# Kernel tuning notes

Measured on AMD Instinct MI355X. Metric: run time of the kernel, lower is better.

## Reference

```python
import jax, jax.numpy as jnp
import numpy as np

B, L, P, K, D, H = 8192, 224, 6, 5, 128, 4
S = K * K                 # 25 spatial positions in the patch
CENTER = S // 2           # central target pixel index
SCALE_RANGE = 0.2
BN_EPS = 1e-5


def _uniform(k, shape, fan_in):
    s = 1.0 / np.sqrt(fan_in)
    return jax.random.uniform(k, shape, jnp.float32, -s, s)


def setup_inputs() -> dict:
    key = jax.random.key(0)
    ks = jax.random.split(key, 32)
    inp = {}
    inp["x"] = jax.random.normal(ks[0], (B, L, K, K), jnp.float32)
    # attention projections (stored as (in, out), applied as x @ W + b)
    inp["wk_w"] = _uniform(ks[1], (L, D), L); inp["wk_b"] = _uniform(ks[2], (D,), L)
    inp["wv_w"] = _uniform(ks[3], (L, D), L); inp["wv_b"] = _uniform(ks[4], (D,), L)
    inp["wq_w"] = _uniform(ks[5], (L, D), L); inp["wq_b"] = _uniform(ks[6], (D,), L)
    inp["ng_w"] = _uniform(ks[7], (D, 1), D); inp["ng_b"] = _uniform(ks[8], (1,), D)
    # ffn branch: GLU(128->64) -> BN -> GLU(64->P)
    inp["f1_fw"] = _uniform(ks[9], (D, 64), D);  inp["f1_fb"] = _uniform(ks[10], (64,), D)
    inp["f1_gw"] = _uniform(ks[11], (D, 64), D); inp["f1_gb"] = _uniform(ks[12], (64,), D)
    inp["f_bn_g"] = jnp.ones((64,), jnp.float32); inp["f_bn_b"] = jnp.zeros((64,), jnp.float32)
    inp["f2_fw"] = _uniform(ks[13], (64, P), 64); inp["f2_fb"] = _uniform(ks[14], (P,), 64)
    inp["f2_gw"] = _uniform(ks[15], (64, P), 64); inp["f2_gb"] = _uniform(ks[16], (P,), 64)
    # scalar branch: same shapes
    inp["s1_fw"] = _uniform(ks[17], (D, 64), D);  inp["s1_fb"] = _uniform(ks[18], (64,), D)
    inp["s1_gw"] = _uniform(ks[19], (D, 64), D);  inp["s1_gb"] = _uniform(ks[20], (64,), D)
    inp["s_bn_g"] = jnp.ones((64,), jnp.float32); inp["s_bn_b"] = jnp.zeros((64,), jnp.float32)
    inp["s2_fw"] = _uniform(ks[21], (64, P), 64); inp["s2_fb"] = _uniform(ks[22], (P,), 64)
    inp["s2_gw"] = _uniform(ks[23], (64, P), 64); inp["s2_gb"] = _uniform(ks[24], (P,), 64)
    # endmember spectra (P, L), nonnegative as typical for HSI
    inp["endmember"] = jax.random.uniform(ks[25], (P, L), jnp.float32)
    return inp


def _swish(x):
    return x * jax.nn.sigmoid(x)


def _glu(x, fw, fb, gw, gb):
    return (x @ fw + fb) * jax.nn.sigmoid(x @ gw + gb)


def _bn_train(x, g, b):
    # BatchNorm1d training-mode forward: biased batch stats over batch dim
    m = jnp.mean(x, axis=0)
    v = jnp.var(x, axis=0)
    return (x - m) * jax.lax.rsqrt(v + BN_EPS) * g + b


def _forward(x, wk_w, wk_b, wv_w, wv_b, wq_w, wq_b, ng_w, ng_b,
             f1_fw, f1_fb, f1_gw, f1_gb, f_bn_g, f_bn_b, f2_fw, f2_fb, f2_gw, f2_gb,
             s1_fw, s1_fb, s1_gw, s1_gb, s_bn_g, s_bn_b, s2_fw, s2_fb, s2_gw, s2_gb,
             endmember):
    b = x.shape[0]
    xt = x.reshape(b, L, S).transpose(0, 2, 1)        # (B, S, L)
    keys = xt @ wk_w + wk_b                            # (B, S, D)
    vals = xt @ wv_w + wv_b                            # (B, S, D)
    q = xt[:, CENTER] @ wq_w + wq_b                    # (B, D)
    dk, dv = D // H, D // H
    kh = keys.reshape(b, S, H, dk)
    qh = q.reshape(b, H, dk)
    # note: scaling uses full key_dim (np.sqrt(self.key_dim)), not per-head dim
    scores = jnp.einsum('bhd,bshd->bhs', qh, kh) / np.sqrt(D).astype(np.float32)
    mask = jnp.zeros((S,), jnp.float32).at[CENTER].set(-1e6)
    att = jax.nn.softmax(scores + mask, axis=-1)       # (B, H, S)
    vh = vals.reshape(b, S, H, dv)
    surround = jnp.einsum('bhs,bshd->bhd', att, vh).reshape(b, D)
    central = vals[:, CENTER]                          # (B, D)
    nearby = jax.nn.sigmoid((central - surround) @ ng_w + ng_b)  # (B, 1)
    ss = central + nearby * surround                   # (B, D) spatial-spectral feature

    h = _glu(_swish(ss), f1_fw, f1_fb, f1_gw, f1_gb)
    h = _swish(_bn_train(h, f_bn_g, f_bn_b))
    abd = jax.nn.softmax(_glu(h, f2_fw, f2_fb, f2_gw, f2_gb), axis=1)  # (B, P)

    g = _glu(_swish(ss), s1_fw, s1_fb, s1_gw, s1_gb)
    g = _swish(_bn_train(g, s_bn_g, s_bn_b))
    edm_scale = jnp.tanh(_glu(g, s2_fw, s2_fb, s2_gw, s2_gb))          # (B, P)

    scale = 1.0 + SCALE_RANGE * edm_scale[:, :, None]  # (B, P, 1)
    edm = scale * endmember[None]                      # (B, P, L)
    recon = jnp.einsum('bp,bpl->bl', abd, edm)         # (B, L)
    return recon, abd, edm_scale


def reference(x, wk_w, wk_b, wv_w, wv_b, wq_w, wq_b, ng_w, ng_b,
              f1_fw, f1_fb, f1_gw, f1_gb, f_bn_g, f_bn_b, f2_fw, f2_fb, f2_gw, f2_gb,
              s1_fw, s1_fb, s1_gw, s1_gb, s_bn_g, s_bn_b, s2_fw, s2_fb, s2_gw, s2_gb,
              endmember):
    return _forward(x, wk_w, wk_b, wv_w, wv_b, wq_w, wq_b, ng_w, ng_b,
                    f1_fw, f1_fb, f1_gw, f1_gb, f_bn_g, f_bn_b, f2_fw, f2_fb, f2_gw, f2_gb,
                    s1_fw, s1_fb, s1_gw, s1_gb, s_bn_g, s_bn_b, s2_fw, s2_fb, s2_gw, s2_gb,
                    endmember)
```

## Files before the change

kernel.cpp:

```cpp
#include <hip/hip_runtime.h>
#include <hip/hip_bf16.h>

typedef unsigned short ushort;
typedef unsigned int   uint;
typedef __bf16 bfrag_t __attribute__((ext_vector_type(8)));
typedef float  ffrag_t __attribute__((ext_vector_type(4)));

#define NB   8192
#define LL   224
#define SS   25
#define CTR  12
#define DD   128
#define PP   6
#define HID  64
#define GPB  2
#define NKC  7
#define NMT  4
#define NNT  24
#define VST  132
#define WPK_ELEMS (NKC * NNT * 64 * 8)
#define FC1_ELEMS (4 * 16 * 64 * 8)

__device__ __forceinline__ float f_sigmoid(float x) { return 1.0f / (1.0f + __expf(-x)); }
__device__ __forceinline__ ushort f2bf(float f) {
    __hip_bfloat16 h = __float2bfloat16(f);
    ushort u; __builtin_memcpy(&u, &h, 2); return u;
}
__device__ __forceinline__ float bfu2f(ushort u) {
    uint v = ((uint)u) << 16; float f; __builtin_memcpy(&f, &v, 4); return f;
}

__global__ __launch_bounds__(256) void k0_pack(
    const float* __restrict__ wk_w, const float* __restrict__ wv_w,
    const float* __restrict__ wq_w,
    const float* __restrict__ f1_fw, const float* __restrict__ f1_gw,
    const float* __restrict__ s1_fw, const float* __restrict__ s1_gw,
    ushort* __restrict__ wpack, ushort* __restrict__ fc1pack)
{
    const int blk = blockIdx.x;
    if (blk < NNT) {
        const int nt  = blk;
        const int mat = nt >> 3;
        const float* w = mat == 0 ? wk_w : (mat == 1 ? wv_w : wq_w);
        const int cb = (nt & 7) * 16;
        for (int e = threadIdx.x; e < NKC * 64 * 8; e += 256) {
            int j    = e & 7;
            int lane = (e >> 3) & 63;
            int kc   = e >> 9;
            int k = kc * 32 + ((lane >> 4) << 3) + j;
            int c = cb + (lane & 15);
            wpack[((kc * NNT + nt) * 64 + lane) * 8 + j] = f2bf(w[k * DD + c]);
        }
    } else {
        const int nt = blk - NNT;
        const int m2 = nt >> 2;
        const float* w = m2 == 0 ? f1_fw : (m2 == 1 ? f1_gw : (m2 == 2 ? s1_fw : s1_gw));
        const int cb = (nt & 3) * 16;
        for (int e = threadIdx.x; e < 4 * 64 * 8; e += 256) {
            int j    = e & 7;
            int lane = (e >> 3) & 63;
            int kc   = e >> 9;
            int k = kc * 32 + ((lane >> 4) << 3) + j;
            int c = cb + (lane & 15);
            fc1pack[((kc * 16 + nt) * 64 + lane) * 8 + j] = f2bf(w[k * HID + c]);
        }
    }
}

__global__ __launch_bounds__(512, 4) void kA_front(
    const float* __restrict__ x,
    const ushort* __restrict__ wpack,
    const float* __restrict__ wk_b, const float* __restrict__ wv_b,
    const float* __restrict__ wq_b,
    const float* __restrict__ ng_w, const float* __restrict__ ng_b,
    ushort* __restrict__ swv_ws)
{
    __shared__ ushort alds[NMT * NKC * 64 * 8];
    __shared__ float  qv[GPB * DD];
    __shared__ float  att[8 * 26];
    __shared__ float  red[4];

    const int t    = threadIdx.x;
    const int b0   = blockIdx.x * GPB;
    const int wave = t >> 6;
    const int lane = t & 63;

    for (int g = 0; g < GPB; ++g) {
        const float* xb = x + (size_t)(b0 + g) * (LL * SS);
        for (int i = t; i < LL * SS; i += 512) {
            int l = i / SS;
            int s = i - l * SS;
            int r  = g * 32 + s;
            int idx = (((r >> 4) * NKC + (l >> 5)) * 64 +
                       ((r & 15) | (((l >> 3) & 3) << 4))) * 8 + (l & 7);
            alds[idx] = f2bf(xb[i]);
        }
    }
    __syncthreads();

    ffrag_t acck[NMT], accv[NMT], accq[2];
#pragma unroll
    for (int mt = 0; mt < NMT; ++mt) {
        acck[mt] = ffrag_t{0.f, 0.f, 0.f, 0.f};
        accv[mt] = ffrag_t{0.f, 0.f, 0.f, 0.f};
    }
    accq[0] = ffrag_t{0.f, 0.f, 0.f, 0.f};
    accq[1] = ffrag_t{0.f, 0.f, 0.f, 0.f};

    for (int kc = 0; kc < NKC; ++kc) {
        bfrag_t bk = *(const bfrag_t*)(wpack + ((kc * NNT + wave) * 64 + lane) * 8);
        bfrag_t bv = *(const bfrag_t*)(wpack + ((kc * NNT + wave + 8) * 64 + lane) * 8);
        bfrag_t bq = *(const bfrag_t*)(wpack + ((kc * NNT + wave + 16) * 64 + lane) * 8);
#pragma unroll
        for (int mt = 0; mt < NMT; ++mt) {
            bfrag_t af = *(const bfrag_t*)(alds + ((mt * NKC + kc) * 64 + lane) * 8);
            acck[mt] = __builtin_amdgcn_mfma_f32_16x16x32_bf16(af, bk, acck[mt], 0, 0, 0);
            accv[mt] = __builtin_amdgcn_mfma_f32_16x16x32_bf16(af, bv, accv[mt], 0, 0, 0);
            if ((mt & 1) == 0)
                accq[mt >> 1] = __builtin_amdgcn_mfma_f32_16x16x32_bf16(af, bq, accq[mt >> 1], 0, 0, 0);
        }
    }
    __syncthreads();

    {
        const int c  = wave * 16 + (lane & 15);
        const float bk = wk_b[c];
        const float bv = wv_b[c];
#pragma unroll
        for (int mt = 0; mt < NMT; ++mt) {
#pragma unroll
            for (int reg = 0; reg < 4; ++reg) {
                int r = mt * 16 + ((lane >> 4) << 2) + reg;
                int g = r >> 5;
                int s = r & 31;
                if (s < SS) {
                    alds[(g * SS + s) * VST + c]        = f2bf(acck[mt][reg] + bk);
                    alds[6600 + (g * SS + s) * VST + c] = f2bf(accv[mt][reg] + bv);
                }
            }
        }
        if ((lane >> 4) == 3) {
            float bq = wq_b[c];
            qv[c]      = accq[0][0] + bq;
            qv[DD + c] = accq[1][0] + bq;
        }
    }
    __syncthreads();

    if (t < 256) {
        const int r   = t >> 5;
        const int g   = r >> 2;
        const int h   = r & 3;
        const int l32 = t & 31;
        float sc = -1e30f;
        if (l32 < SS) {
            const ushort* kr = alds + (g * SS + l32) * VST + h * 32;
            const float*  qr = qv + g * DD + h * 32;
            float a0 = 0.f, a1 = 0.f, a2 = 0.f, a3 = 0.f;
#pragma unroll
            for (int i = 0; i < 32; i += 4) {
                a0 = fmaf(qr[i + 0], bfu2f(kr[i + 0]), a0);
                a1 = fmaf(qr[i + 1], bfu2f(kr[i + 1]), a1);
                a2 = fmaf(qr[i + 2], bfu2f(kr[i + 2]), a2);
                a3 = fmaf(qr[i + 3], bfu2f(kr[i + 3]), a3);
            }
            sc = ((a0 + a1) + (a2 + a3)) * 0.088388347648318447f;
            if (l32 == CTR) sc -= 1e6f;
        }
        float mx = sc;
#pragma unroll
        for (int m = 16; m > 0; m >>= 1) mx = fmaxf(mx, __shfl_xor(mx, m, 32));
        float e = __expf(sc - mx);
        float sum = e;
#pragma unroll
        for (int m = 16; m > 0; m >>= 1) sum += __shfl_xor(sum, m, 32);
        if (l32 < SS) att[r * 26 + l32] = e / sum;
    }
    __syncthreads();

    if (t < 256) {
        const int g = t >> 7;
        const int d = t & 127;
        const int h = d >> 5;
        const ushort* vrow = alds + 6600 + g * SS * VST + d;
        const float* arow = att + (g * 4 + h) * 26;
        float s0 = 0.f, s1 = 0.f;
#pragma unroll
        for (int s = 0; s < 24; s += 2) {
            s0 = fmaf(arow[s],     bfu2f(vrow[s * VST]),       s0);
            s1 = fmaf(arow[s + 1], bfu2f(vrow[(s + 1) * VST]), s1);
        }
        float sur = fmaf(arow[24], bfu2f(vrow[24 * VST]), s0 + s1);
        float cen = bfu2f(vrow[CTR * VST]);
        float term = (cen - sur) * ng_w[d];
#pragma unroll
        for (int off = 32; off > 0; off >>= 1) term += __shfl_down(term, off);
        if (lane == 0) red[wave] = term;
        __syncthreads();
        float tot = red[g * 2] + red[g * 2 + 1] + ng_b[0];
        float nearby = f_sigmoid(tot);
        float ssv = cen + nearby * sur;
        float sw  = ssv * f_sigmoid(ssv);
        swv_ws[(size_t)(b0 + g) * DD + d] = f2bf(sw);
    } else {
        __syncthreads();
    }
}

__global__ __launch_bounds__(256) void kC_fc1(
    const ushort* __restrict__ swv_ws,
    const ushort* __restrict__ fc1pack,
    const float* __restrict__ f1_fb, const float* __restrict__ f1_gb,
    const float* __restrict__ s1_fb, const float* __restrict__ s1_gb,
    float* __restrict__ h1_ws, float* __restrict__ g1_ws)
{
    const int t    = threadIdx.x;
    const int wave = t >> 6;
    const int lane = t & 63;
    const int m0   = blockIdx.x * 32;

    ffrag_t acc[4][2];
#pragma unroll
    for (int ni = 0; ni < 4; ++ni)
#pragma unroll
        for (int mt = 0; mt < 2; ++mt) acc[ni][mt] = ffrag_t{0.f, 0.f, 0.f, 0.f};

#pragma unroll
    for (int kc = 0; kc < 4; ++kc) {
        bfrag_t bf[4];
#pragma unroll
        for (int ni = 0; ni < 4; ++ni) {
            int nt = wave + 4 * ni;
            bf[ni] = *(const bfrag_t*)(fc1pack + ((kc * 16 + nt) * 64 + lane) * 8);
        }
#pragma unroll
        for (int mt = 0; mt < 2; ++mt) {
            bfrag_t af = *(const bfrag_t*)(swv_ws +
                (size_t)(m0 + mt * 16 + (lane & 15)) * DD + kc * 32 + ((lane >> 4) << 3));
#pragma unroll
            for (int ni = 0; ni < 4; ++ni)
                acc[ni][mt] = __builtin_amdgcn_mfma_f32_16x16x32_bf16(af, bf[ni], acc[ni][mt], 0, 0, 0);
        }
    }

    const int c16 = wave * 16 + (lane & 15);
    const float fb1 = f1_fb[c16], gb1 = f1_gb[c16];
    const float fb2 = s1_fb[c16], gb2 = s1_gb[c16];
#pragma unroll
    for (int mt = 0; mt < 2; ++mt) {
#pragma unroll
        for (int reg = 0; reg < 4; ++reg) {
            int m = m0 + mt * 16 + ((lane >> 4) << 2) + reg;
            float hf = acc[0][mt][reg] + fb1;
            float hg = acc[1][mt][reg] + gb1;
            float gf = acc[2][mt][reg] + fb2;
            float gg = acc[3][mt][reg] + gb2;
            h1_ws[(size_t)m * HID + c16] = hf * f_sigmoid(hg);
            g1_ws[(size_t)m * HID + c16] = gf * f_sigmoid(gg);
        }
    }
}

__global__ __launch_bounds__(256) void k2a_part(
    const float* __restrict__ h1, const float* __restrict__ g1,
    float* __restrict__ part)
{
    const int br    = blockIdx.x >> 5;
    const int chunk = blockIdx.x & 31;
    const float* src = br ? g1 : h1;
    const int t = threadIdx.x;
    const int w = t >> 6;
    const int j = t & 63;
    const int base = chunk * 256;
    float s = 0.f, sq = 0.f;
    for (int i = 0; i < 64; ++i) {
        float v = src[(size_t)(base + i * 4 + w) * HID + j];
        s += v;
        sq = fmaf(v, v, sq);
    }
    __shared__ float ls[4][64], lq[4][64];
    ls[w][j] = s; lq[w][j] = sq;
    __syncthreads();
    if (t < 64) {
        float S = ls[0][t] + ls[1][t] + ls[2][t] + ls[3][t];
        float Q = lq[0][t] + lq[1][t] + lq[2][t] + lq[3][t];
        float* pr = part + (br * 32 + chunk) * 128;
        pr[t]      = S;
        pr[64 + t] = Q;
    }
}

__global__ __launch_bounds__(128) void k2b_fin(
    const float* __restrict__ part,
    const float* __restrict__ fg, const float* __restrict__ fb,
    const float* __restrict__ sg, const float* __restrict__ sb,
    float* __restrict__ bn)
{
    const int t = threadIdx.x;
    const int br = t >> 6;
    const int j  = t & 63;
    float S1 = 0.f, S2 = 0.f;
#pragma unroll 8
    for (int c = 0; c < 32; ++c) {
        const float* pr = part + (br * 32 + c) * 128;
        S1 += pr[j];
        S2 += pr[64 + j];
    }
    float m   = S1 * (1.0f / NB);
    float var = S2 * (1.0f / NB) - m * m;
    float g  = br ? sg[j] : fg[j];
    float be = br ? sb[j] : fb[j];
    float a  = g * rsqrtf(var + 1e-5f);
    bn[br * 128 + j]      = a;
    bn[br * 128 + 64 + j] = be - m * a;
}

#define K3G 32
__global__ __launch_bounds__(256) void k3_back(
    const float* __restrict__ h1, const float* __restrict__ g1,
    const float* __restrict__ bn,
    const float* __restrict__ f2_fw, const float* __restrict__ f2_fb,
    const float* __restrict__ f2_gw, const float* __restrict__ f2_gb,
    const float* __restrict__ s2_fw, const float* __restrict__ s2_fb,
    const float* __restrict__ s2_gw, const float* __restrict__ s2_gb,
    const float* __restrict__ endm,
    float* __restrict__ out_recon, float* __restrict__ out_abd,
    float* __restrict__ out_es)
{
    const int B0 = blockIdx.x * K3G;
    const int t = threadIdx.x;
    __shared__ float bnl[256];
    __shared__ float w2[4][HID * PP];
    __shared__ float b2[4][8];
    __shared__ float endl[PP * LL];
    __shared__ float hh[K3G * 65], gg[K3G * 65];
    __shared__ float logit[K3G * 8], esv[K3G * 8], coef[K3G * 8];

    bnl[t] = bn[t];
    for (int i = t; i < HID * PP; i += 256) {
        w2[0][i] = f2_fw[i];
        w2[1][i] = f2_gw[i];
        w2[2][i] = s2_fw[i];
        w2[3][i] = s2_gw[i];
    }
    if (t < PP) {
        b2[0][t] = f2_fb[t];
        b2[1][t] = f2_gb[t];
        b2[2][t] = s2_fb[t];
        b2[3][t] = s2_gb[t];
    }
    for (int i = t; i < PP * LL; i += 256) endl[i] = endm[i];
    __syncthreads();

    for (int i = t; i < K3G * HID; i += 256) {
        int ba = i >> 6, j = i & 63;
        float v1 = h1[(size_t)(B0 + ba) * HID + j] * bnl[j] + bnl[64 + j];
        hh[ba * 65 + j] = v1 * f_sigmoid(v1);
        float v2 = g1[(size_t)(B0 + ba) * HID + j] * bnl[128 + j] + bnl[192 + j];
        gg[ba * 65 + j] = v2 * f_sigmoid(v2);
    }
    __syncthreads();

    for (int i = t; i < K3G * 2 * PP; i += 256) {
        int ba = i / (2 * PP);
        int rr = i - ba * (2 * PP);
        int br = rr / PP;
        int p  = rr - br * PP;
        const float* src = (br ? gg : hh) + ba * 65;
        const float* fw  = w2[br * 2];
        const float* gw  = w2[br * 2 + 1];
        float df = b2[br * 2][p], dg = b2[br * 2 + 1][p];
#pragma unroll 8
        for (int j = 0; j < HID; ++j) {
            float v = src[j];
            df = fmaf(v, fw[j * PP + p], df);
            dg = fmaf(v, gw[j * PP + p], dg);
        }
        float glu = df * f_sigmoid(dg);
        if (br == 0) {
            logit[ba * 8 + p] = glu;
        } else {
            float e = tanhf(glu);
            esv[ba * 8 + p] = e;
            out_es[(size_t)(B0 + ba) * PP + p] = e;
        }
    }
    __syncthreads();

    if (t < K3G) {
        float mx = -1e30f;
#pragma unroll
        for (int p = 0; p < PP; ++p) mx = fmaxf(mx, logit[t * 8 + p]);
        float e[PP]; float sum = 0.f;
#pragma unroll
        for (int p = 0; p < PP; ++p) { e[p] = __expf(logit[t * 8 + p] - mx); sum += e[p]; }
        float inv = 1.0f / sum;
#pragma unroll
        for (int p = 0; p < PP; ++p) {
            float a = e[p] * inv;
            out_abd[(size_t)(B0 + t) * PP + p] = a;
            coef[t * 8 + p] = a * (1.0f + 0.2f * esv[t * 8 + p]);
        }
    }
    __syncthreads();

    for (int i = t; i < K3G * LL; i += 256) {
        int ba = i / LL;
        int l  = i - ba * LL;
        float r = 0.f;
#pragma unroll
        for (int p = 0; p < PP; ++p)
            r = fmaf(coef[ba * 8 + p], endl[p * LL + l], r);
        out_recon[(size_t)(B0 + ba) * LL + l] = r;
    }
}

extern "C" void kernel_launch(void* const* d_in, const int* in_sizes, int n_in,
                              void* d_out, int out_size, void* d_ws, size_t ws_size,
                              hipStream_t stream)
{
    const float* x     = (const float*)d_in[0];
    const float* wk_w  = (const float*)d_in[1];
    const float* wk_b  = (const float*)d_in[2];
    const float* wv_w  = (const float*)d_in[3];
    const float* wv_b  = (const float*)d_in[4];
    const float* wq_w  = (const float*)d_in[5];
    const float* wq_b  = (const float*)d_in[6];
    const float* ng_w  = (const float*)d_in[7];
    const float* ng_b  = (const float*)d_in[8];
    const float* f1_fw = (const float*)d_in[9];
    const float* f1_fb = (const float*)d_in[10];
    const float* f1_gw = (const float*)d_in[11];
    const float* f1_gb = (const float*)d_in[12];
    const float* f_bng = (const float*)d_in[13];
    const float* f_bnb = (const float*)d_in[14];
    const float* f2_fw = (const float*)d_in[15];
    const float* f2_fb = (const float*)d_in[16];
    const float* f2_gw = (const float*)d_in[17];
    const float* f2_gb = (const float*)d_in[18];
    const float* s1_fw = (const float*)d_in[19];
    const float* s1_fb = (const float*)d_in[20];
    const float* s1_gw = (const float*)d_in[21];
    const float* s1_gb = (const float*)d_in[22];
    const float* s_bng = (const float*)d_in[23];
    const float* s_bnb = (const float*)d_in[24];
    const float* s2_fw = (const float*)d_in[25];
    const float* s2_fb = (const float*)d_in[26];
    const float* s2_gw = (const float*)d_in[27];
    const float* s2_gb = (const float*)d_in[28];
    const float* endm  = (const float*)d_in[29];

    float* ws = (float*)d_ws;
    float*  h1_ws   = ws;
    float*  g1_ws   = ws + (size_t)NB * HID;
    float*  bn      = ws + 1048576;
    float*  part    = ws + 1048832;
    ushort* wpack   = (ushort*)(ws + 1057024);
    ushort* fc1pack = (ushort*)(ws + 1057024 + WPK_ELEMS / 2);
    ushort* swv_ws  = (ushort*)(ws + 1057024 + (WPK_ELEMS + FC1_ELEMS) / 2);

    float* out       = (float*)d_out;
    float* out_recon = out;
    float* out_abd   = out + (size_t)NB * LL;
    float* out_es    = out + (size_t)NB * (LL + PP);

    k0_pack<<<NNT + 16, 256, 0, stream>>>(wk_w, wv_w, wq_w, f1_fw, f1_gw,
                                          s1_fw, s1_gw, wpack, fc1pack);
    kA_front<<<NB / GPB, 512, 0, stream>>>(x, wpack, wk_b, wv_b, wq_b,
                                           ng_w, ng_b, swv_ws);
    kC_fc1<<<NB / 32, 256, 0, stream>>>(swv_ws, fc1pack, f1_fb, f1_gb,
                                        s1_fb, s1_gb, h1_ws, g1_ws);
    k2a_part<<<64, 256, 0, stream>>>(h1_ws, g1_ws, part);
    k2b_fin<<<1, 128, 0, stream>>>(part, f_bng, f_bnb, s_bng, s_bnb, bn);
    k3_back<<<NB / K3G, 256, 0, stream>>>(h1_ws, g1_ws, bn,
                                          f2_fw, f2_fb, f2_gw, f2_gb,
                                          s2_fw, s2_fb, s2_gw, s2_gb,
                                          endm, out_recon, out_abd, out_es);
}
```

Measured before the change: 405.5 us.

## Fuse BN statistics into fc1 via atomics, vectorize x loads, prefetch weights

Batch-norm sum and sum-of-squares are now accumulated inside the fc1 kernel with wave shuffles and global atomics. This removes the two separate reduction kernels, and the final scale/shift is computed at the start of the back kernel. The stats buffer is zeroed in the pack kernel. The front kernel now loads x as float4 into registers before scattering to LDS, and double-buffers the weight fragments across k-chunks, with bias loads hoisted early. Atomics add contention and make the summation order nondeterministic.

Result: faster. 369.5 us (-8.9%).

```diff
diff --git a/kernel.cpp b/kernel.cpp
--- a/kernel.cpp
+++ b/kernel.cpp
@@ -35,9 +35,11 @@
     const float* __restrict__ wq_w,
     const float* __restrict__ f1_fw, const float* __restrict__ f1_gw,
     const float* __restrict__ s1_fw, const float* __restrict__ s1_gw,
-    ushort* __restrict__ wpack, ushort* __restrict__ fc1pack)
+    ushort* __restrict__ wpack, ushort* __restrict__ fc1pack,
+    float* __restrict__ stats)
 {
     const int blk = blockIdx.x;
+    if (blk == 0) stats[threadIdx.x] = 0.f;
     if (blk < NNT) {
         const int nt  = blk;
         const int mat = nt >> 3;
@@ -85,15 +87,37 @@
     const int wave = t >> 6;
     const int lane = t & 63;
 
-    for (int g = 0; g < GPB; ++g) {
-        const float* xb = x + (size_t)(b0 + g) * (LL * SS);
-        for (int i = t; i < LL * SS; i += 512) {
-            int l = i / SS;
-            int s = i - l * SS;
-            int r  = g * 32 + s;
-            int idx = (((r >> 4) * NKC + (l >> 5)) * 64 +
-                       ((r & 15) | (((l >> 3) & 3) << 4))) * 8 + (l & 7);
-            alds[idx] = f2bf(xb[i]);
+    const int cC = wave * 16 + (lane & 15);
+    const float biask = wk_b[cC];
+    const float biasv = wv_b[cC];
+    const float biasq = wq_b[cC];
+    const float ngw   = ng_w[t & 127];
+
+    const float4* xb4 = (const float4*)(x + (size_t)b0 * (LL * SS));
+    float4 xf[6];
+#pragma unroll
+    for (int k = 0; k < 6; ++k) {
+        int q = t + k * 512;
+        if (q < 2800) xf[k] = xb4[q];
+    }
+#pragma unroll
+    for (int k = 0; k < 6; ++k) {
+        int q = t + k * 512;
+        if (q < 2800) {
+            int e0 = q * 4;
+            int g  = e0 >= 5600;
+            int eb0 = e0 - g * 5600;
+#pragma unroll
+            for (int c = 0; c < 4; ++c) {
+                int eb = eb0 + c;
+                int l = eb / 25;
+                int s = eb - l * 25;
+                int r = g * 32 + s;
+                int idx = (((r >> 4) * NKC + (l >> 5)) * 64 +
+                           ((r & 15) | (((l >> 3) & 3) << 4))) * 8 + (l & 7);
+                float fv = c == 0 ? xf[k].x : c == 1 ? xf[k].y : c == 2 ? xf[k].z : xf[k].w;
+                alds[idx] = f2bf(fv);
+            }
         }
     }
     __syncthreads();
@@ -107,10 +131,17 @@
     accq[0] = ffrag_t{0.f, 0.f, 0.f, 0.f};
     accq[1] = ffrag_t{0.f, 0.f, 0.f, 0.f};
 
+    bfrag_t bk = *(const bfrag_t*)(wpack + ((0 * NNT + wave) * 64 + lane) * 8);
+    bfrag_t bv = *(const bfrag_t*)(wpack + ((0 * NNT + wave + 8) * 64 + lane) * 8);
+    bfrag_t bq = *(const bfrag_t*)(wpack + ((0 * NNT + wave + 16) * 64 + lane) * 8);
+#pragma unroll
     for (int kc = 0; kc < NKC; ++kc) {
-        bfrag_t bk = *(const bfrag_t*)(wpack + ((kc * NNT + wave) * 64 + lane) * 8);
-        bfrag_t bv = *(const bfrag_t*)(wpack + ((kc * NNT + wave + 8) * 64 + lane) * 8);
-        bfrag_t bq = *(const bfrag_t*)(wpack + ((kc * NNT + wave + 16) * 64 + lane) * 8);
+        bfrag_t nbk, nbv, nbq;
+        if (kc + 1 < NKC) {
+            nbk = *(const bfrag_t*)(wpack + (((kc + 1) * NNT + wave) * 64 + lane) * 8);
+            nbv = *(const bfrag_t*)(wpack + (((kc + 1) * NNT + wave + 8) * 64 + lane) * 8);
+            nbq = *(const bfrag_t*)(wpack + (((kc + 1) * NNT + wave + 16) * 64 + lane) * 8);
+        }
 #pragma unroll
         for (int mt = 0; mt < NMT; ++mt) {
             bfrag_t af = *(const bfrag_t*)(alds + ((mt * NKC + kc) * 64 + lane) * 8);
@@ -119,13 +150,11 @@
             if ((mt & 1) == 0)
                 accq[mt >> 1] = __builtin_amdgcn_mfma_f32_16x16x32_bf16(af, bq, accq[mt >> 1], 0, 0, 0);
         }
+        if (kc + 1 < NKC) { bk = nbk; bv = nbv; bq = nbq; }
     }
     __syncthreads();
 
     {
-        const int c  = wave * 16 + (lane & 15);
-        const float bk = wk_b[c];
-        const float bv = wv_b[c];
 #pragma unroll
         for (int mt = 0; mt < NMT; ++mt) {
 #pragma unroll
@@ -134,15 +163,14 @@
                 int g = r >> 5;
                 int s = r & 31;
                 if (s < SS) {
-                    alds[(g * SS + s) * VST + c]        = f2bf(acck[mt][reg] + bk);
-                    alds[6600 + (g * SS + s) * VST + c] = f2bf(accv[mt][reg] + bv);
+                    alds[(g * SS + s) * VST + cC]        = f2bf(acck[mt][reg] + biask);
+                    alds[6600 + (g * SS + s) * VST + cC] = f2bf(accv[mt][reg] + biasv);
                 }
             }
         }
         if ((lane >> 4) == 3) {
-            float bq = wq_b[c];
-            qv[c]      = accq[0][0] + bq;
-            qv[DD + c] = accq[1][0] + bq;
+            qv[cC]      = accq[0][0] + biasq;
+            qv[DD + cC] = accq[1][0] + biasq;
         }
     }
     __syncthreads();
@@ -192,7 +220,7 @@
         }
         float sur = fmaf(arow[24], bfu2f(vrow[24 * VST]), s0 + s1);
         float cen = bfu2f(vrow[CTR * VST]);
-        float term = (cen - sur) * ng_w[d];
+        float term = (cen - sur) * ngw;
 #pragma unroll
         for (int off = 32; off > 0; off >>= 1) term += __shfl_down(term, off);
         if (lane == 0) red[wave] = term;
@@ -212,12 +240,17 @@
     const ushort* __restrict__ fc1pack,
     const float* __restrict__ f1_fb, const float* __restrict__ f1_gb,
     const float* __restrict__ s1_fb, const float* __restrict__ s1_gb,
-    float* __restrict__ h1_ws, float* __restrict__ g1_ws)
+    float* __restrict__ h1_ws, float* __restrict__ g1_ws,
+    float* __restrict__ stats)
 {
     const int t    = threadIdx.x;
     const int wave = t >> 6;
     const int lane = t & 63;
     const int m0   = blockIdx.x * 32;
+    const int c16  = wave * 16 + (lane & 15);
+
+    const float fb1 = f1_fb[c16], gb1 = f1_gb[c16];
+    const float fb2 = s1_fb[c16], gb2 = s1_gb[c16];
 
     ffrag_t acc[4][2];
 #pragma unroll
@@ -243,82 +276,35 @@
         }
     }
 
-    const int c16 = wave * 16 + (lane & 15);
-    const float fb1 = f1_fb[c16], gb1 = f1_gb[c16];
-    const float fb2 = s1_fb[c16], gb2 = s1_gb[c16];
+    float hs = 0.f, hq = 0.f, gs = 0.f, gq = 0.f;
 #pragma unroll
     for (int mt = 0; mt < 2; ++mt) {
 #pragma unroll
         for (int reg = 0; reg < 4; ++reg) {
             int m = m0 + mt * 16 + ((lane >> 4) << 2) + reg;
-            float hf = acc[0][mt][reg] + fb1;
-            float hg = acc[1][mt][reg] + gb1;
-            float gf = acc[2][mt][reg] + fb2;
-            float gg = acc[3][mt][reg] + gb2;
-            h1_ws[(size_t)m * HID + c16] = hf * f_sigmoid(hg);
-            g1_ws[(size_t)m * HID + c16] = gf * f_sigmoid(gg);
-        }
-    }
-}
-
-__global__ __launch_bounds__(256) void k2a_part(
-    const float* __restrict__ h1, const float* __restrict__ g1,
-    float* __restrict__ part)
-{
-    const int br    = blockIdx.x >> 5;
-    const int chunk = blockIdx.x & 31;
-    const float* src = br ? g1 : h1;
-    const int t = threadIdx.x;
-    const int w = t >> 6;
-    const int j = t & 63;
-    const int base = chunk * 256;
-    float s = 0.f, sq = 0.f;
-    for (int i = 0; i < 64; ++i) {
-        float v = src[(size_t)(base + i * 4 + w) * HID + j];
-        s += v;
-        sq = fmaf(v, v, sq);
-    }
-    __shared__ float ls[4][64], lq[4][64];
-    ls[w][j] = s; lq[w][j] = sq;
-    __syncthreads();
-    if (t < 64) {
-        float S = ls[0][t] + ls[1][t] + ls[2][t] + ls[3][t];
-        float Q = lq[0][t] + lq[1][t] + lq[2][t] + lq[3][t];
-        float* pr = part + (br * 32 + chunk) * 128;
-        pr[t]      = S;
-        pr[64 + t] = Q;
-    }
-}
-
-__global__ __launch_bounds__(128) void k2b_fin(
-    const float* __restrict__ part,
-    const float* __restrict__ fg, const float* __restrict__ fb,
-    const float* __restrict__ sg, const float* __restrict__ sb,
-    float* __restrict__ bn)
-{
-    const int t = threadIdx.x;
-    const int br = t >> 6;
-    const int j  = t & 63;
-    float S1 = 0.f, S2 = 0.f;
-#pragma unroll 8
-    for (int c = 0; c < 32; ++c) {
-        const float* pr = part + (br * 32 + c) * 128;
-        S1 += pr[j];
-        S2 += pr[64 + j];
-    }
-    float m   = S1 * (1.0f / NB);
-    float var = S2 * (1.0f / NB) - m * m;
-    float g  = br ? sg[j] : fg[j];
-    float be = br ? sb[j] : fb[j];
-    float a  = g * rsqrtf(var + 1e-5f);
-    bn[br * 128 + j]      = a;
-    bn[br * 128 + 64 + j] = be - m * a;
+            float hv = (acc[0][mt][reg] + fb1) * f_sigmoid(acc[1][mt][reg] + gb1);
+            float gv = (acc[2][mt][reg] + fb2) * f_sigmoid(acc[3][mt][reg] + gb2);
+            h1_ws[(size_t)m * HID + c16] = hv;
+            g1_ws[(size_t)m * HID + c16] = gv;
+            hs += hv; hq = fmaf(hv, hv, hq);
+            gs += gv; gq = fmaf(gv, gv, gq);
+        }
+    }
+    hs += __shfl_xor(hs, 16); hs += __shfl_xor(hs, 32);
+    hq += __shfl_xor(hq, 16); hq += __shfl_xor(hq, 32);
+    gs += __shfl_xor(gs, 16); gs += __shfl_xor(gs, 32);
+    gq += __shfl_xor(gq, 16); gq += __shfl_xor(gq, 32);
+    const int cg = lane >> 4;
+    float val = cg == 0 ? hs : cg == 1 ? hq : cg == 2 ? gs : gq;
+    atomicAdd(&stats[cg * 64 + c16], val);
 }
 
 #define K3G 32
 __global__ __launch_bounds__(256) void k3_back(
     const float* __restrict__ h1, const float* __restrict__ g1,
-    const float* __restrict__ bn,
+    const float* __restrict__ stats,
+    const float* __restrict__ f_bng, const float* __restrict__ f_bnb,
+    const float* __restrict__ s_bng, const float* __restrict__ s_bnb,
     const float* __restrict__ f2_fw, const float* __restrict__ f2_fb,
     const float* __restrict__ f2_gw, const float* __restrict__ f2_gb,
     const float* __restrict__ s2_fw, const float* __restrict__ s2_fb,
@@ -336,7 +322,18 @@
     __shared__ float hh[K3G * 65], gg[K3G * 65];
     __shared__ float logit[K3G * 8], esv[K3G * 8], coef[K3G * 8];
 
-    bnl[t] = bn[t];
+    if (t < 128) {
+        int br = t >> 6, j = t & 63;
+        float S1 = stats[br * 128 + j];
+        float S2 = stats[br * 128 + 64 + j];
+        float m   = S1 * (1.0f / NB);
+        float var = S2 * (1.0f / NB) - m * m;
+        float gam = br ? s_bng[j] : f_bng[j];
+        float be  = br ? s_bnb[j] : f_bnb[j];
+        float a   = gam * rsqrtf(var + 1e-5f);
+        bnl[br * 128 + j]      = a;
+        bnl[br * 128 + 64 + j] = be - m * a;
+    }
     for (int i = t; i < HID * PP; i += 256) {
         w2[0][i] = f2_fw[i];
         w2[1][i] = f2_gw[i];
@@ -453,11 +450,10 @@
     float* ws = (float*)d_ws;
     float*  h1_ws   = ws;
     float*  g1_ws   = ws + (size_t)NB * HID;
-    float*  bn      = ws + 1048576;
-    float*  part    = ws + 1048832;
-    ushort* wpack   = (ushort*)(ws + 1057024);
-    ushort* fc1pack = (ushort*)(ws + 1057024 + WPK_ELEMS / 2);
-    ushort* swv_ws  = (ushort*)(ws + 1057024 + (WPK_ELEMS + FC1_ELEMS) / 2);
+    float*  stats   = ws + 1048576;
+    ushort* wpack   = (ushort*)(ws + 1048832);
+    ushort* fc1pack = (ushort*)(ws + 1048832 + WPK_ELEMS / 2);
+    ushort* swv_ws  = (ushort*)(ws + 1048832 + (WPK_ELEMS + FC1_ELEMS) / 2);
 
     float* out       = (float*)d_out;
     float* out_recon = out;
@@ -465,14 +461,13 @@
     float* out_es    = out + (size_t)NB * (LL + PP);
 
     k0_pack<<<NNT + 16, 256, 0, stream>>>(wk_w, wv_w, wq_w, f1_fw, f1_gw,
-                                          s1_fw, s1_gw, wpack, fc1pack);
+                                          s1_fw, s1_gw, wpack, fc1pack, stats);
     kA_front<<<NB / GPB, 512, 0, stream>>>(x, wpack, wk_b, wv_b, wq_b,
                                            ng_w, ng_b, swv_ws);
     kC_fc1<<<NB / 32, 256, 0, stream>>>(swv_ws, fc1pack, f1_fb, f1_gb,
-                                        s1_fb, s1_gb, h1_ws, g1_ws);
-    k2a_part<<<64, 256, 0, stream>>>(h1_ws, g1_ws, part);
-    k2b_fin<<<1, 128, 0, stream>>>(part, f_bng, f_bnb, s_bng, s_bnb, bn);
-    k3_back<<<NB / K3G, 256, 0, stream>>>(h1_ws, g1_ws, bn,
+                                        s1_fb, s1_gb, h1_ws, g1_ws, stats);
+    k3_back<<<NB / K3G, 256, 0, stream>>>(h1_ws, g1_ws, stats,
+                                          f_bng, f_bnb, s_bng, s_bnb,
                                           f2_fw, f2_fb, f2_gw, f2_gb,
                                           s2_fw, s2_fb, s2_gw, s2_gb,
                                           endm, out_recon, out_abd, out_es);
```
